# Optimization experiments

Measured on AMD Instinct MI355X. Metric: run time of the kernel, lower is better.

## Reference

```python
import jax, jax.numpy as jnp
import numpy as np


def setup_inputs() -> dict:
    key = jax.random.key(0)
    ks = jax.random.split(key, 8)
    B, C, D, H, W = 4, 256, 16, 16, 16
    C8 = C // 8
    x = jax.random.normal(ks[0], (B, C, D, H, W), dtype=jnp.float32)
    # 1x1x1 conv weights == per-channel linear maps
    Wq = jax.random.normal(ks[1], (C8, C), dtype=jnp.float32) * (1.0 / np.sqrt(C))
    bq = jax.random.normal(ks[2], (C8,), dtype=jnp.float32) * 0.01
    Wk = jax.random.normal(ks[3], (C8, C), dtype=jnp.float32) * (1.0 / np.sqrt(C))
    bk = jax.random.normal(ks[4], (C8,), dtype=jnp.float32) * 0.01
    Wv = jax.random.normal(ks[5], (C, C), dtype=jnp.float32) * (1.0 / np.sqrt(C))
    bv = jax.random.normal(ks[6], (C,), dtype=jnp.float32) * 0.01
    gamma = jax.random.normal(ks[7], (1,), dtype=jnp.float32) * 0.1
    return {"x": x, "Wq": Wq, "bq": bq, "Wk": Wk, "bk": bk,
            "Wv": Wv, "bv": bv, "gamma": gamma}


def reference(x, Wq, bq, Wk, bk, Wv, bv, gamma):
    B, C, D, H, W = x.shape
    N = D * H * W
    xf = x.reshape(B, C, N)  # (B, C, N)
    # 1x1x1 convs == channel-wise linear projections
    q = jnp.einsum('qc,bcn->bnq', Wq, xf) + bq            # (B, N, C/8)
    k = jnp.einsum('kc,bcn->bkn', Wk, xf) + bk[:, None]   # (B, C/8, N)
    v = jnp.einsum('vc,bcn->bvn', Wv, xf) + bv[:, None]   # (B, C, N)
    energy = jnp.einsum('bnc,bcm->bnm', q, k)             # (B, N, N), NO 1/sqrt(d) scaling (as in source)
    attention = jax.nn.softmax(energy, axis=-1)           # softmax over keys
    # out[b,c,m] = sum_n V[b,c,n] * A[b,m,n]  (torch: bmm(V, A^T))
    out = jnp.einsum('bcn,bmn->bcm', v, attention)        # (B, C, N)
    out = out.reshape(B, C, D, H, W)
    return gamma[0] * out + x
```

## Files before the change

### kernel.cpp

```cpp
#include <hip/hip_runtime.h>
#include <hip/hip_bf16.h>
#include <math.h>

#define BATCH 4
#define CH    256
#define NPOS  4096
#define DQK   32
#define LOG2E 1.4426950408889634f
#define QB2   (-28.853900817779268f)

typedef __attribute__((ext_vector_type(8))) short bf16x8;
typedef __attribute__((ext_vector_type(4))) float f32x4;

static __device__ __forceinline__ unsigned int pack_bf2(float a, float b) {
    __hip_bfloat162 h = __float22bfloat162_rn(make_float2(a, b));
    return *reinterpret_cast<unsigned int*>(&h);
}
static __device__ __forceinline__ unsigned short f2bf1(float f) {
    unsigned int u = __float_as_uint(f);
    u += 0x7fff + ((u >> 16) & 1);
    return (unsigned short)(u >> 16);
}

static __device__ __forceinline__ void lds_barrier() {
    asm volatile("s_waitcnt lgkmcnt(0)" ::: "memory");
    __builtin_amdgcn_s_barrier();
    asm volatile("" ::: "memory");
}

__global__ __launch_bounds__(256) void conv_w(
    const float* __restrict__ Wq, const float* __restrict__ bq,
    const float* __restrict__ Wk, const float* __restrict__ bk,
    const float* __restrict__ Wv, const float* __restrict__ bv,
    __hip_bfloat16* __restrict__ Wbf, float* __restrict__ bcat)
{
    const int co = blockIdx.x;
    const int ci = threadIdx.x;
    const float* src; float scale = 1.f;
    if (co < 32)      { src = Wq + (size_t)co * 256;        scale = LOG2E; }
    else if (co < 64) { src = Wk + (size_t)(co - 32) * 256; }
    else              { src = Wv + (size_t)(co - 64) * 256; }
    *reinterpret_cast<unsigned short*>(Wbf + (size_t)co * 256 + ci) =
        f2bf1(src[ci] * scale);
    if (ci == 0)
        bcat[co] = co < 32 ? bq[co] * LOG2E
                 : (co < 64 ? bk[co - 32] : bv[co - 64]);
}

__global__ __launch_bounds__(256) void qkv_proj_mfma(
    const float* __restrict__ x,
    const __hip_bfloat16* __restrict__ Wbf, const float* __restrict__ bcat,
    __hip_bfloat16* __restrict__ qb, __hip_bfloat16* __restrict__ kb,
    __hip_bfloat16* __restrict__ vb)
{
    __shared__ alignas(16) unsigned char Xl[16384];
    const int tid  = threadIdx.x;
    const int wave = tid >> 6, lane = tid & 63;
    const int g    = lane >> 4, lm = lane & 15;
    const int n0   = blockIdx.x * 32;
    const int b    = blockIdx.y;

    {
        const int c   = tid;
        const int ktc = c >> 5, gc = (c >> 3) & 3, jc = c & 7;
        const unsigned xw = (unsigned)(4 * ktc + gc);
        const float* xp = x + ((size_t)b * CH + c) * NPOS + n0;
        #pragma unroll
        for (int i = 0; i < 8; ++i) {
            const float4 v4 = reinterpret_cast<const float4*>(xp)[i];
            const float vv[4] = {v4.x, v4.y, v4.z, v4.w};
            #pragma unroll
            for (int e = 0; e < 4; ++e) {
                const int nrel = 4 * i + e;
                const unsigned off =
                    (unsigned)(((nrel >> 4) * 8 + ktc) * 1024)
                  + ((((unsigned)(gc * 16 + (nrel & 15))) ^ xw) * 16)
                  + (unsigned)(jc * 2);
                *reinterpret_cast<unsigned short*>(Xl + off) = f2bf1(vv[e]);
            }
        }
    }
    __syncthreads();

    bf16x8 xf[2][8];
    #pragma unroll
    for (int nt = 0; nt < 2; ++nt)
        #pragma unroll
        for (int kt = 0; kt < 8; ++kt) {
            const unsigned slot = (unsigned)lane ^ (unsigned)(4 * kt + g);
            xf[nt][kt] = *reinterpret_cast<const bf16x8*>(
                Xl + (unsigned)((nt * 8 + kt) * 1024) + slot * 16);
        }

    #pragma unroll
    for (int s = 0; s < 5; ++s) {
        const int cot = wave * 5 + s;
        const int cog = cot * 16;

        bf16x8 wf[8];
        const __hip_bfloat16* wrow = Wbf + (size_t)(cog + lm) * 256;
        #pragma unroll
        for (int kt = 0; kt < 8; ++kt)
            wf[kt] = *reinterpret_cast<const bf16x8*>(wrow + 32 * kt + 8 * g);

        const float4 b4 = *reinterpret_cast<const float4*>(bcat + cog + 4 * g);
        f32x4 a0 = {b4.x, b4.y, b4.z, b4.w};
        f32x4 a1 = a0;
        #pragma unroll
        for (int kt = 0; kt < 8; ++kt) {
            a0 = __builtin_amdgcn_mfma_f32_16x16x32_bf16(wf[kt], xf[0][kt], a0, 0, 0, 0);
            a1 = __builtin_amdgcn_mfma_f32_16x16x32_bf16(wf[kt], xf[1][kt], a1, 0, 0, 0);
        }

        if (cot < 4) {
            __hip_bfloat16* dst = (cot < 2 ? qb : kb);
            const int cb = (cot < 2 ? cot * 16 : cot * 16 - 32);
            #pragma unroll
            for (int nt = 0; nt < 2; ++nt) {
                f32x4 a = nt ? a1 : a0;
                int n = n0 + 16 * nt + lm;
                uint2 w;
                w.x = pack_bf2(a[0], a[1]);
                w.y = pack_bf2(a[2], a[3]);
                *(uint2*)(dst + ((size_t)b * NPOS + n) * DQK + cb + 4 * g) = w;
            }
        } else {
            const int cbase = cot * 16 - 64;
            #pragma unroll
            for (int nt = 0; nt < 2; ++nt) {
                f32x4 a = nt ? a1 : a0;
                int n = n0 + 16 * nt + lm;
                int n64 = n >> 6, half = (n >> 5) & 1, nin = n & 31;
                #pragma unroll
                for (int r = 0; r < 4; ++r) {
                    int c = cbase + 4 * g + r;
                    size_t off = (((size_t)b * 16 + (c >> 4)) * 64 + n64) * 1024
                               + (size_t)half * 512 + (c & 15) * 32 + nin;
                    *reinterpret_cast<unsigned short*>(vb + off) = f2bf1(a[r]);
                }
            }
        }
    }
}

__global__ __launch_bounds__(512) void flash_pam_kernel(
    const __hip_bfloat16* __restrict__ qb, const __hip_bfloat16* __restrict__ kb,
    const __hip_bfloat16* __restrict__ vb, const float* __restrict__ x,
    const float* __restrict__ gamma, float* __restrict__ out)
{
    __shared__ alignas(16) unsigned char Pl[2][8192];
    __shared__ float lred[4][4][16];

    const int tid  = threadIdx.x;
    const int wave = tid >> 6;
    const int lane = tid & 63;
    const int g    = lane >> 4;
    const int lm   = lane & 15;
    const int bid  = blockIdx.x;
    const int b    = bid & 3;
    const int m0   = (bid >> 2) * 64;
    const int kt   = wave & 3;
    const int mtA  = (wave >> 2) * 2;
    const unsigned swz = (unsigned)(lm & 7) << 4;

    const bf16x8 qfA = *reinterpret_cast<const bf16x8*>(
        qb + ((size_t)b * NPOS + m0 + 16 * mtA + lm) * DQK + 8 * g);
    const bf16x8 qfB = *reinterpret_cast<const bf16x8*>(
        qb + ((size_t)b * NPOS + m0 + 16 * mtA + 16 + lm) * DQK + 8 * g);

    const __hip_bfloat16* kbb = kb + (size_t)b * NPOS * DQK;
    const int koff0 = (16 * kt + lm) * DQK + 8 * g;
    const __hip_bfloat16* vbb = vb + (size_t)b * 16 * 64 * 1024;
    int vfb[4];
    #pragma unroll
    for (int cti = 0; cti < 2; ++cti)
        #pragma unroll
        for (int kc = 0; kc < 2; ++kc)
            vfb[2 * cti + kc] = (2 * wave + cti) * 65536 + kc * 512 + lm * 32 + 8 * g;

    const unsigned wbA = (unsigned)(16 * mtA + lm) * 128
                       + (((unsigned)(32 * kt + 8 * g)) ^ swz);
    const unsigned wbB = wbA + 16 * 128;

    unsigned char* P0 = &Pl[0][0];
    unsigned char* P1 = &Pl[1][0];

    f32x4 acc[2][4];
    #pragma unroll
    for (int i = 0; i < 2; ++i)
        #pragma unroll
        for (int j = 0; j < 4; ++j) acc[i][j] = (f32x4){0.f, 0.f, 0.f, 0.f};
    float lsA = 0.f, lsB = 0.f;

#define LOADK(dst, tk_) \
    dst = *reinterpret_cast<const bf16x8*>(kbb + koff0 + (tk_) * 2048);

#define LOADV(dst, tv_) { \
    _Pragma("unroll") for (int f = 0; f < 4; ++f) \
        dst[f] = *reinterpret_cast<const bf16x8*>(vbb + vfb[f] + (tv_) * 1024); }

#define QKW(KU, PW) { \
    f32x4 zb = {QB2, QB2, QB2, QB2}; \
    f32x4 sA = __builtin_amdgcn_mfma_f32_16x16x32_bf16(KU, qfA, zb, 0, 0, 0); \
    f32x4 sB = __builtin_amdgcn_mfma_f32_16x16x32_bf16(KU, qfB, zb, 0, 0, 0); \
    { float p0 = exp2f(sA[0]), p1 = exp2f(sA[1]); \
      float p2 = exp2f(sA[2]), p3 = exp2f(sA[3]); \
      lsA += (p0 + p1) + (p2 + p3); \
      uint2 w; w.x = pack_bf2(p0, p1); w.y = pack_bf2(p2, p3); \
      *reinterpret_cast<uint2*>((PW) + wbA) = w; } \
    { float p0 = exp2f(sB[0]), p1 = exp2f(sB[1]); \
      float p2 = exp2f(sB[2]), p3 = exp2f(sB[3]); \
      lsB += (p0 + p1) + (p2 + p3); \
      uint2 w; w.x = pack_bf2(p0, p1); w.y = pack_bf2(p2, p3); \
      *reinterpret_cast<uint2*>((PW) + wbB) = w; } }

#define PVt(PR, VR) { \
    _Pragma("unroll") for (int kc = 0; kc < 2; ++kc) { \
        bf16x8 pf[4]; \
        _Pragma("unroll") for (int mt = 0; mt < 4; ++mt) \
            pf[mt] = *reinterpret_cast<const bf16x8*>( \
                (PR) + (unsigned)(16 * mt + lm) * 128 \
                     + (((unsigned)(kc * 64 + 16 * g)) ^ swz)); \
        __builtin_amdgcn_s_setprio(1); \
        _Pragma("unroll") for (int cti = 0; cti < 2; ++cti) \
            _Pragma("unroll") for (int mt = 0; mt < 4; ++mt) \
                acc[cti][mt] = __builtin_amdgcn_mfma_f32_16x16x32_bf16( \
                    VR[2 * cti + kc], pf[mt], acc[cti][mt], 0, 0, 0); \
        __builtin_amdgcn_s_setprio(0); } }

#define BODY(t_, PR, PW, VR, VL, KU, KL) { \
    { int tv = (t_) + 1; if (tv > 63) tv = 63; LOADV(VL, tv); } \
    { int tk2 = (t_) + 2; if (tk2 > 63) tk2 = 63; LOADK(KL, tk2); } \
    __builtin_amdgcn_sched_barrier(0); \
    QKW(KU, PW); \
    PVt(PR, VR); \
    lds_barrier(); }

    bf16x8 kA, kB, vA[4], vB[4];
    LOADK(kA, 0);
    LOADV(vA, 0);
    LOADK(kB, 1);
    __builtin_amdgcn_sched_barrier(0);
    QKW(kA, P0);
    lds_barrier();

    for (int it = 0; it < 31; ++it) {
        BODY(2 * it,     P0, P1, vA, vB, kB, kA);
        BODY(2 * it + 1, P1, P0, vB, vA, kA, kB);
    }
    BODY(62, P0, P1, vA, vB, kB, kA);
    PVt(P1, vB);

    lsA += __shfl_xor(lsA, 16); lsA += __shfl_xor(lsA, 32);
    lsB += __shfl_xor(lsB, 16); lsB += __shfl_xor(lsB, 32);
    if (lane < 16) {
        lred[kt][mtA][lm]     = lsA;
        lred[kt][mtA + 1][lm] = lsB;
    }
    __syncthreads();

    float linv[4];
    #pragma unroll
    for (int mt = 0; mt < 4; ++mt)
        linv[mt] = 1.f / (lred[0][mt][lm] + lred[1][mt][lm]
                        + lred[2][mt][lm] + lred[3][mt][lm]);

    const float gmv = gamma[0];
    #pragma unroll
    for (int cti = 0; cti < 2; ++cti)
        #pragma unroll
        for (int mt = 0; mt < 4; ++mt)
            #pragma unroll
            for (int r = 0; r < 4; ++r) {
                int c = 32 * wave + 16 * cti + 4 * g + r;
                size_t idx = ((size_t)b * CH + c) * NPOS + m0 + 16 * mt + lm;
                out[idx] = gmv * (acc[cti][mt][r] * linv[mt]) + x[idx];
            }
#undef BODY
#undef PVt
#undef QKW
#undef LOADV
#undef LOADK
}

extern "C" void kernel_launch(void* const* d_in, const int* in_sizes, int n_in,
                              void* d_out, int out_size, void* d_ws, size_t ws_size,
                              hipStream_t stream) {
    const float* x  = (const float*)d_in[0];
    const float* Wq = (const float*)d_in[1];
    const float* bq = (const float*)d_in[2];
    const float* Wk = (const float*)d_in[3];
    const float* bk = (const float*)d_in[4];
    const float* Wv = (const float*)d_in[5];
    const float* bv = (const float*)d_in[6];
    const float* gm = (const float*)d_in[7];
    float* out = (float*)d_out;

    __hip_bfloat16* qbuf = (__hip_bfloat16*)d_ws;
    __hip_bfloat16* kbuf = qbuf + (size_t)BATCH * NPOS * DQK;
    __hip_bfloat16* vbuf = kbuf + (size_t)BATCH * NPOS * DQK;
    __hip_bfloat16* wbf  = vbuf + (size_t)BATCH * CH * NPOS;
    float* bcat = (float*)(wbf + 320 * 256);

    conv_w<<<dim3(320), 256, 0, stream>>>(Wq, bq, Wk, bk, Wv, bv, wbf, bcat);
    qkv_proj_mfma<<<dim3(NPOS / 32, BATCH), 256, 0, stream>>>(
        x, wbf, bcat, qbuf, kbuf, vbuf);
    flash_pam_kernel<<<dim3(NPOS / 64 * BATCH), 512, 0, stream>>>(
        qbuf, kbuf, vbuf, x, gm, out);
}
```

Baseline: 72.96 us.

## Repartition PV work per wave to 64 channels by 32 queries

Changes the P·V tile owned by each wave from 32 channels by 64 queries to 64 channels by 32 queries, so each wave reads only the two P tiles matching its own query half from LDS. This halves LDS reads of P per wave but doubles V fragment loads from global memory and the V register footprint per wave. It also drops the explicit scheduling barriers so the compiler can interleave loads with the QK and softmax work. Register pressure rises and could hurt occupancy at 512 threads.

```diff
diff --git a/kernel.cpp b/kernel.cpp
--- a/kernel.cpp
+++ b/kernel.cpp
@@ -160,7 +160,9 @@
     const int b    = bid & 3;
     const int m0   = (bid >> 2) * 64;
     const int kt   = wave & 3;
-    const int mtA  = (wave >> 2) * 2;
+    const int mhalf= wave >> 2;
+    const int mtA  = mhalf * 2;
+    const int cq   = wave & 3;
     const unsigned swz = (unsigned)(lm & 7) << 4;
 
     const bf16x8 qfA = *reinterpret_cast<const bf16x8*>(
@@ -171,12 +173,12 @@
     const __hip_bfloat16* kbb = kb + (size_t)b * NPOS * DQK;
     const int koff0 = (16 * kt + lm) * DQK + 8 * g;
     const __hip_bfloat16* vbb = vb + (size_t)b * 16 * 64 * 1024;
-    int vfb[4];
-    #pragma unroll
-    for (int cti = 0; cti < 2; ++cti)
+    int vfb[8];
+    #pragma unroll
+    for (int ct = 0; ct < 4; ++ct)
         #pragma unroll
         for (int kc = 0; kc < 2; ++kc)
-            vfb[2 * cti + kc] = (2 * wave + cti) * 65536 + kc * 512 + lm * 32 + 8 * g;
+            vfb[2 * ct + kc] = (4 * cq + ct) * 65536 + kc * 512 + lm * 32 + 8 * g;
 
     const unsigned wbA = (unsigned)(16 * mtA + lm) * 128
                        + (((unsigned)(32 * kt + 8 * g)) ^ swz);
@@ -185,18 +187,18 @@
     unsigned char* P0 = &Pl[0][0];
     unsigned char* P1 = &Pl[1][0];
 
-    f32x4 acc[2][4];
-    #pragma unroll
-    for (int i = 0; i < 2; ++i)
-        #pragma unroll
-        for (int j = 0; j < 4; ++j) acc[i][j] = (f32x4){0.f, 0.f, 0.f, 0.f};
+    f32x4 acc[4][2];
+    #pragma unroll
+    for (int i = 0; i < 4; ++i)
+        #pragma unroll
+        for (int j = 0; j < 2; ++j) acc[i][j] = (f32x4){0.f, 0.f, 0.f, 0.f};
     float lsA = 0.f, lsB = 0.f;
 
 #define LOADK(dst, tk_) \
     dst = *reinterpret_cast<const bf16x8*>(kbb + koff0 + (tk_) * 2048);
 
 #define LOADV(dst, tv_) { \
-    _Pragma("unroll") for (int f = 0; f < 4; ++f) \
+    _Pragma("unroll") for (int f = 0; f < 8; ++f) \
         dst[f] = *reinterpret_cast<const bf16x8*>(vbb + vfb[f] + (tv_) * 1024); }
 
 #define QKW(KU, PW) { \
@@ -216,31 +218,29 @@
 
 #define PVt(PR, VR) { \
     _Pragma("unroll") for (int kc = 0; kc < 2; ++kc) { \
-        bf16x8 pf[4]; \
-        _Pragma("unroll") for (int mt = 0; mt < 4; ++mt) \
-            pf[mt] = *reinterpret_cast<const bf16x8*>( \
-                (PR) + (unsigned)(16 * mt + lm) * 128 \
+        bf16x8 pf[2]; \
+        _Pragma("unroll") for (int mtl = 0; mtl < 2; ++mtl) \
+            pf[mtl] = *reinterpret_cast<const bf16x8*>( \
+                (PR) + (unsigned)(16 * (mtA + mtl) + lm) * 128 \
                      + (((unsigned)(kc * 64 + 16 * g)) ^ swz)); \
         __builtin_amdgcn_s_setprio(1); \
-        _Pragma("unroll") for (int cti = 0; cti < 2; ++cti) \
-            _Pragma("unroll") for (int mt = 0; mt < 4; ++mt) \
-                acc[cti][mt] = __builtin_amdgcn_mfma_f32_16x16x32_bf16( \
-                    VR[2 * cti + kc], pf[mt], acc[cti][mt], 0, 0, 0); \
+        _Pragma("unroll") for (int ct = 0; ct < 4; ++ct) \
+            _Pragma("unroll") for (int mtl = 0; mtl < 2; ++mtl) \
+                acc[ct][mtl] = __builtin_amdgcn_mfma_f32_16x16x32_bf16( \
+                    VR[2 * ct + kc], pf[mtl], acc[ct][mtl], 0, 0, 0); \
         __builtin_amdgcn_s_setprio(0); } }
 
 #define BODY(t_, PR, PW, VR, VL, KU, KL) { \
     { int tv = (t_) + 1; if (tv > 63) tv = 63; LOADV(VL, tv); } \
     { int tk2 = (t_) + 2; if (tk2 > 63) tk2 = 63; LOADK(KL, tk2); } \
-    __builtin_amdgcn_sched_barrier(0); \
     QKW(KU, PW); \
     PVt(PR, VR); \
     lds_barrier(); }
 
-    bf16x8 kA, kB, vA[4], vB[4];
+    bf16x8 kA, kB, vA[8], vB[8];
     LOADK(kA, 0);
     LOADV(vA, 0);
     LOADK(kB, 1);
-    __builtin_amdgcn_sched_barrier(0);
     QKW(kA, P0);
     lds_barrier();
 
@@ -259,22 +259,25 @@
     }
     __syncthreads();
 
-    float linv[4];
-    #pragma unroll
-    for (int mt = 0; mt < 4; ++mt)
-        linv[mt] = 1.f / (lred[0][mt][lm] + lred[1][mt][lm]
-                        + lred[2][mt][lm] + lred[3][mt][lm]);
+    float linv[2];
+    #pragma unroll
+    for (int mtl = 0; mtl < 2; ++mtl) {
+        const int mt = mtA + mtl;
+        linv[mtl] = 1.f / (lred[0][mt][lm] + lred[1][mt][lm]
+                         + lred[2][mt][lm] + lred[3][mt][lm]);
+    }
 
     const float gmv = gamma[0];
     #pragma unroll
-    for (int cti = 0; cti < 2; ++cti)
-        #pragma unroll
-        for (int mt = 0; mt < 4; ++mt)
+    for (int ct = 0; ct < 4; ++ct)
+        #pragma unroll
+        for (int mtl = 0; mtl < 2; ++mtl)
             #pragma unroll
             for (int r = 0; r < 4; ++r) {
-                int c = 32 * wave + 16 * cti + 4 * g + r;
-                size_t idx = ((size_t)b * CH + c) * NPOS + m0 + 16 * mt + lm;
-                out[idx] = gmv * (acc[cti][mt][r] * linv[mt]) + x[idx];
+                int c = 64 * cq + 16 * ct + 4 * g + r;
+                size_t idx = ((size_t)b * CH + c) * NPOS
+                           + m0 + 16 * (mtA + mtl) + lm;
+                out[idx] = gmv * (acc[ct][mtl][r] * linv[mtl]) + x[idx];
             }
 #undef BODY
 #undef PVt
```

Measured after the change: 94.57 us. 1.3x slower.
